# Kernel optimization log

Hardware: AMD Instinct MI355X
Metric: run time of the kernel (lower is better)

The kernel has to match this reference:

```python
import jax, jax.numpy as jnp
import numpy as np

B, S, C = 64, 1024, 512
EPS = 1e-5

def setup_inputs() -> dict:
    key = jax.random.key(0)
    k1, k2, k3 = jax.random.split(key, 3)
    x = jax.random.normal(k1, (B, S, C), dtype=jnp.float32)
    # LayerNorm affine over normalized_shape=[S, C]
    ln_w = jnp.ones((S, C), dtype=jnp.float32)
    ln_b = jnp.zeros((S, C), dtype=jnp.float32)
    # Linear(seq_len, seq_len): torch init U(-1/sqrt(S), 1/sqrt(S))
    bound = 1.0 / np.sqrt(S)
    lin_w = jax.random.uniform(k2, (S, S), jnp.float32, -bound, bound)
    lin_b = jax.random.uniform(k3, (S,), jnp.float32, -bound, bound)
    return {"x": x, "ln_w": ln_w, "ln_b": ln_b, "lin_w": lin_w, "lin_b": lin_b}

def reference(x, ln_w, ln_b, lin_w, lin_b):
    # LayerNorm over last two dims [S, C]
    mu = jnp.mean(x, axis=(1, 2), keepdims=True)
    var = jnp.mean(jnp.square(x - mu), axis=(1, 2), keepdims=True)
    h = (x - mu) * jax.lax.rsqrt(var + EPS) * ln_w + ln_b
    # permute -> [B, C, S], linear over S, relu, permute back, residual
    # fused as einsum over the seq axis directly (no explicit transpose)
    y = jnp.einsum('bsc,ts->btc', h, lin_w) + lin_b[None, :, None]
    y = jax.nn.relu(y)
    return x + y
```

## Files before the change

kernel.cpp:

```cpp
#include <hip/hip_runtime.h>
#include <stdint.h>

#define BB 64
#define SS 1024
#define CC 512
#define EPS 1e-5f

typedef __attribute__((ext_vector_type(8))) __bf16 bf16x8;
typedef __attribute__((ext_vector_type(8))) unsigned short ushort8v;
typedef __attribute__((ext_vector_type(4))) float f32x4;

__device__ __forceinline__ unsigned short f2bf(float f) {
    unsigned int u = __builtin_bit_cast(unsigned int, f);
    u += 0x7fffu + ((u >> 16) & 1u);
    return (unsigned short)(u >> 16);
}

__global__ __launch_bounds__(256) void k_prep(const float* __restrict__ x,
                                              const float* __restrict__ lnw,
                                              const float* __restrict__ lnb,
                                              const float* __restrict__ linw,
                                              unsigned short* __restrict__ Wb,
                                              unsigned short* __restrict__ Ht,
                                              float* __restrict__ psum,
                                              float* __restrict__ psq) {
    const int id = blockIdx.x;
    const int t = threadIdx.x;
    if (id >= 8448) {
        int i = (id - 8448) * 256 + t;
        float4 v = ((const float4*)linw)[i];
        ushort4 o;
        o.x = f2bf(v.x); o.y = f2bf(v.y); o.z = f2bf(v.z); o.w = f2bf(v.w);
        ((ushort4*)Wb)[i] = o;
        return;
    }
    __shared__ uint32_t lds[64 * 33];
    __shared__ float ls[4], lq[4];
    int b, rem;
    const float* src;
    const float* wp;
    if (id < 8192)      { b = id >> 7; rem = id & 127; src = x + (size_t)b * SS * CC; wp = lnw; }
    else if (id < 8320) { b = 64; rem = id - 8192; src = lnw; wp = nullptr; }
    else                { b = 65; rem = id - 8320; src = lnb; wp = nullptr; }
    const int s0 = (rem >> 3) << 6;
    const int c0 = (rem & 7) << 6;
    const int cq = t & 15, spA = t >> 4;
    float sA = 0.f, qA = 0.f;
#pragma unroll
    for (int h = 0; h < 2; ++h) {
        int sp = spA + h * 16;
        int sl = s0 + 2 * sp;
        int cc = c0 + 4 * cq;
        size_t xb = (size_t)sl * CC + cc;
        float4 a0 = *(const float4*)(src + xb);
        float4 a1 = *(const float4*)(src + xb + CC);
        float4 g0 = a0, g1 = a1;
        if (wp) {
            float4 w0 = *(const float4*)(wp + xb);
            float4 w1 = *(const float4*)(wp + xb + CC);
            g0.x = a0.x * w0.x; g0.y = a0.y * w0.y; g0.z = a0.z * w0.z; g0.w = a0.w * w0.w;
            g1.x = a1.x * w1.x; g1.y = a1.y * w1.y; g1.z = a1.z * w1.z; g1.w = a1.w * w1.w;
            sA += a0.x + a0.y + a0.z + a0.w + a1.x + a1.y + a1.z + a1.w;
            qA += a0.x*a0.x + a0.y*a0.y + a0.z*a0.z + a0.w*a0.w
                + a1.x*a1.x + a1.y*a1.y + a1.z*a1.z + a1.w*a1.w;
        }
        uint32_t u0 = (uint32_t)f2bf(g0.x) | ((uint32_t)f2bf(g1.x) << 16);
        uint32_t u1 = (uint32_t)f2bf(g0.y) | ((uint32_t)f2bf(g1.y) << 16);
        uint32_t u2 = (uint32_t)f2bf(g0.z) | ((uint32_t)f2bf(g1.z) << 16);
        uint32_t u3 = (uint32_t)f2bf(g0.w) | ((uint32_t)f2bf(g1.w) << 16);
        lds[(4 * cq + 0) * 33 + sp] = u0;
        lds[(4 * cq + 1) * 33 + sp] = u1;
        lds[(4 * cq + 2) * 33 + sp] = u2;
        lds[(4 * cq + 3) * 33 + sp] = u3;
    }
    if (wp) {
        for (int off = 32; off; off >>= 1) {
            sA += __shfl_down(sA, off, 64);
            qA += __shfl_down(qA, off, 64);
        }
        if ((t & 63) == 0) { ls[t >> 6] = sA; lq[t >> 6] = qA; }
    }
    __syncthreads();
    int spq = t & 7, clA = t >> 3;
#pragma unroll
    for (int h = 0; h < 2; ++h) {
        int cl = clA + h * 32;
        uint4 v;
        v.x = lds[cl * 33 + spq * 4 + 0];
        v.y = lds[cl * 33 + spq * 4 + 1];
        v.z = lds[cl * 33 + spq * 4 + 2];
        v.w = lds[cl * 33 + spq * 4 + 3];
        size_t o = (((size_t)b * CC + c0 + cl) * SS + (size_t)s0 + spq * 8) >> 3;
        ((uint4*)Ht)[o] = v;
    }
    if (wp && t == 0) {
        psum[id] = ls[0] + ls[1] + ls[2] + ls[3];
        psq[id]  = lq[0] + lq[1] + lq[2] + lq[3];
    }
}

__global__ __launch_bounds__(128) void k_stats2(const float* __restrict__ psum,
                                                const float* __restrict__ psq,
                                                float* __restrict__ mu,
                                                float* __restrict__ rsg) {
    int b = blockIdx.x, t = threadIdx.x;
    float s = psum[b * 128 + t];
    float q = psq[b * 128 + t];
    for (int off = 32; off; off >>= 1) {
        s += __shfl_down(s, off, 64);
        q += __shfl_down(q, off, 64);
    }
    __shared__ float ls[2], lq[2];
    if ((t & 63) == 0) { ls[t >> 6] = s; lq[t >> 6] = q; }
    __syncthreads();
    if (t == 0) {
        float ss = ls[0] + ls[1], qq = lq[0] + lq[1];
        const float inv = 1.f / (float)(SS * CC);
        float m = ss * inv;
        float v = qq * inv - m * m;
        mu[b] = m;
        rsg[b] = rsqrtf(v + EPS);
    }
}

template<bool FINAL>
__global__ __launch_bounds__(256) void k_gemm(const unsigned short* __restrict__ A,
                                              const unsigned short* __restrict__ Htall,
                                              const float* __restrict__ x,
                                              const float* __restrict__ linb,
                                              const float* __restrict__ wl,
                                              const float* __restrict__ blp,
                                              const float* __restrict__ muA,
                                              const float* __restrict__ rsA,
                                              float* __restrict__ out) {
    int b, tm, tn;
    if constexpr (FINAL) {
        int wg = ((blockIdx.x & 7) << 8) | (blockIdx.x >> 3);
        b = wg >> 5;
        int r2 = wg & 31;
        tm = r2 >> 2; tn = r2 & 3;
    } else {
        tn = blockIdx.x; tm = blockIdx.y; b = 64 + blockIdx.z;
    }
    __shared__ __align__(16) unsigned short SM[16384];
    const int tid = threadIdx.x;
    const int lane = tid & 63;
    const int w = tid >> 6;
    const int wm = w >> 1, wn = w & 1;
    const int quad = lane >> 4, l15 = lane & 15;

    f32x4 acc[4][4];
#pragma unroll
    for (int mi = 0; mi < 4; ++mi)
#pragma unroll
        for (int ni = 0; ni < 4; ++ni)
            acc[mi][ni] = (f32x4){0.f, 0.f, 0.f, 0.f};

    const unsigned short* Ab = A + (size_t)(tm * 128) * 1024;
    const unsigned short* Bb = Htall + ((size_t)b * 512 + tn * 128) * 1024;
    const int srow = tid >> 2;
    const int scol = (tid & 3) * 8;

    auto stage = [&](int buf, int k0) {
#pragma unroll
        for (int q = 0; q < 2; ++q) {
            __builtin_amdgcn_global_load_lds(
                (const __attribute__((address_space(1))) void*)(Ab + (size_t)(q * 64 + srow) * 1024 + k0 + scol),
                (__attribute__((address_space(3))) void*)(SM + buf * 4096 + q * 2048 + w * 512),
                16, 0, 0);
            __builtin_amdgcn_global_load_lds(
                (const __attribute__((address_space(1))) void*)(Bb + (size_t)(q * 64 + srow) * 1024 + k0 + scol),
                (__attribute__((address_space(3))) void*)(SM + 8192 + buf * 4096 + q * 2048 + w * 512),
                16, 0, 0);
        }
    };
    auto compute = [&](int buf) {
        const unsigned short* as = SM + buf * 4096;
        const unsigned short* bs = SM + 8192 + buf * 4096;
        bf16x8 av[4], bv[4];
#pragma unroll
        for (int i = 0; i < 4; ++i) {
            ushort8v a  = *(const ushort8v*)&as[(wm * 64 + i * 16 + l15) * 32 + quad * 8];
            ushort8v b2 = *(const ushort8v*)&bs[(wn * 64 + i * 16 + l15) * 32 + quad * 8];
            av[i] = __builtin_bit_cast(bf16x8, a);
            bv[i] = __builtin_bit_cast(bf16x8, b2);
        }
#pragma unroll
        for (int mi = 0; mi < 4; ++mi)
#pragma unroll
            for (int ni = 0; ni < 4; ++ni)
                acc[mi][ni] = __builtin_amdgcn_mfma_f32_16x16x32_bf16(
                    av[mi], bv[ni], acc[mi][ni], 0, 0, 0);
    };

    stage(0, 0);
    __syncthreads();
    for (int j = 0; j < 15; ++j) {
        int k0 = j * 64;
        stage(1, k0 + 32);
        compute(0);
        __syncthreads();
        stage(0, k0 + 64);
        compute(1);
        __syncthreads();
    }
    stage(1, 992);
    compute(0);
    __syncthreads();
    compute(1);

    if constexpr (FINAL) {
        __syncthreads();
        const float rsv  = rsA[b];
        const float rsmu = rsv * muA[b];
        float* eps = (float*)SM + (w << 11);
#pragma unroll
        for (int ch = 0; ch < 2; ++ch) {
#pragma unroll
            for (int m2 = 0; m2 < 2; ++m2) {
                int mi = ch * 2 + m2;
#pragma unroll
                for (int ni = 0; ni < 4; ++ni)
#pragma unroll
                    for (int r = 0; r < 4; ++r)
                        eps[(m2 * 16 + quad * 4 + r) * 64 + ni * 16 + l15] = acc[mi][ni][r];
            }
#pragma unroll
            for (int jj = 0; jj < 8; ++jj) {
                int row = jj * 4 + quad;
                int tt = tm * 128 + wm * 64 + ch * 32 + row;
                int cc = tn * 128 + wn * 64 + l15 * 4;
                size_t o2 = (size_t)tt * 512 + cc;
                size_t o  = ((size_t)b * 1024 + tt) * 512 + cc;
                f32x4 v   = *(f32x4*)&eps[row * 64 + l15 * 4];
                f32x4 wv  = *(const f32x4*)&wl[o2];
                f32x4 bv2 = *(const f32x4*)&blp[o2];
                f32x4 xv  = *(const f32x4*)&x[o];
                f32x4 ov;
#pragma unroll
                for (int e = 0; e < 4; ++e) {
                    float vv = rsv * v[e] - rsmu * wv[e] + bv2[e];
                    vv = vv > 0.f ? vv : 0.f;
                    ov[e] = xv[e] + vv;
                }
                *(f32x4*)&out[o] = ov;
            }
        }
    } else {
        int z = b - 64;
#pragma unroll
        for (int mi = 0; mi < 4; ++mi) {
#pragma unroll
            for (int r = 0; r < 4; ++r) {
                int tt = tm * 128 + wm * 64 + mi * 16 + quad * 4 + r;
                float add = z ? linb[tt] : 0.f;
#pragma unroll
                for (int ni = 0; ni < 4; ++ni) {
                    int cc = tn * 128 + wn * 64 + ni * 16 + l15;
                    out[((size_t)z * 1024 + tt) * 512 + cc] = acc[mi][ni][r] + add;
                }
            }
        }
    }
}

extern "C" void kernel_launch(void* const* d_in, const int* in_sizes, int n_in,
                              void* d_out, int out_size, void* d_ws, size_t ws_size,
                              hipStream_t stream) {
    (void)in_sizes; (void)n_in; (void)out_size; (void)ws_size;
    const float* x    = (const float*)d_in[0];
    const float* lnw  = (const float*)d_in[1];
    const float* lnb  = (const float*)d_in[2];
    const float* linw = (const float*)d_in[3];
    const float* linb = (const float*)d_in[4];
    float* out = (float*)d_out;

    char* ws = (char*)d_ws;
    unsigned short* Wb = (unsigned short*)ws;
    unsigned short* Ht = (unsigned short*)(ws + (2u << 20));
    float* wlblp = (float*)(ws + (68u << 20));
    float* psum  = (float*)(ws + (72u << 20));
    float* psq   = psum + 8192;
    float* mu    = psq + 8192;
    float* rsg   = mu + 64;

    k_prep<<<9472, 256, 0, stream>>>(x, lnw, lnb, linw, Wb, Ht, psum, psq);
    k_stats2<<<64, 128, 0, stream>>>(psum, psq, mu, rsg);
    k_gemm<false><<<dim3(4, 8, 2), 256, 0, stream>>>(Wb, Ht, nullptr, linb,
                                                     nullptr, nullptr, nullptr, nullptr, wlblp);
    k_gemm<true><<<2048, 256, 0, stream>>>(Wb, Ht, x, nullptr,
                                           wlblp, wlblp + 512 * 1024, mu, rsg, out);
}
```

Baseline: 395.0 us.

## Triple-buffer GEMM K-loop, swizzle LDS, store epilogue terms in bf16, remap XCD tiles

```diff
diff --git a/kernel.cpp b/kernel.cpp
--- a/kernel.cpp
+++ b/kernel.cpp
@@ -14,6 +14,9 @@
     unsigned int u = __builtin_bit_cast(unsigned int, f);
     u += 0x7fffu + ((u >> 16) & 1u);
     return (unsigned short)(u >> 16);
+}
+__device__ __forceinline__ float bf2f(unsigned short u) {
+    return __builtin_bit_cast(float, (uint32_t)u << 16);
 }
 
 __global__ __launch_bounds__(256) void k_prep(const float* __restrict__ x,
@@ -128,21 +131,22 @@
                                               const unsigned short* __restrict__ Htall,
                                               const float* __restrict__ x,
                                               const float* __restrict__ linb,
-                                              const float* __restrict__ wl,
-                                              const float* __restrict__ blp,
+                                              const unsigned short* __restrict__ wlb,
+                                              const unsigned short* __restrict__ blb,
                                               const float* __restrict__ muA,
                                               const float* __restrict__ rsA,
                                               float* __restrict__ out) {
     int b, tm, tn;
     if constexpr (FINAL) {
-        int wg = ((blockIdx.x & 7) << 8) | (blockIdx.x >> 3);
-        b = wg >> 5;
-        int r2 = wg & 31;
-        tm = r2 >> 2; tn = r2 & 3;
+        int xcd = blockIdx.x & 7;
+        int local = blockIdx.x >> 3;
+        b = xcd * 8 + (local >> 5);
+        tn = (local >> 3) & 3;
+        tm = local & 7;
     } else {
         tn = blockIdx.x; tm = blockIdx.y; b = 64 + blockIdx.z;
     }
-    __shared__ __align__(16) unsigned short SM[16384];
+    __shared__ __align__(16) unsigned short SM[24576];
     const int tid = threadIdx.x;
     const int lane = tid & 63;
     const int w = tid >> 6;
@@ -159,29 +163,30 @@
     const unsigned short* Ab = A + (size_t)(tm * 128) * 1024;
     const unsigned short* Bb = Htall + ((size_t)b * 512 + tn * 128) * 1024;
     const int srow = tid >> 2;
-    const int scol = (tid & 3) * 8;
+    const int scol = ((tid & 3) ^ ((srow >> 1) & 3)) * 8;
 
     auto stage = [&](int buf, int k0) {
 #pragma unroll
         for (int q = 0; q < 2; ++q) {
             __builtin_amdgcn_global_load_lds(
                 (const __attribute__((address_space(1))) void*)(Ab + (size_t)(q * 64 + srow) * 1024 + k0 + scol),
-                (__attribute__((address_space(3))) void*)(SM + buf * 4096 + q * 2048 + w * 512),
+                (__attribute__((address_space(3))) void*)(SM + buf * 8192 + q * 2048 + w * 512),
                 16, 0, 0);
             __builtin_amdgcn_global_load_lds(
                 (const __attribute__((address_space(1))) void*)(Bb + (size_t)(q * 64 + srow) * 1024 + k0 + scol),
-                (__attribute__((address_space(3))) void*)(SM + 8192 + buf * 4096 + q * 2048 + w * 512),
+                (__attribute__((address_space(3))) void*)(SM + buf * 8192 + 4096 + q * 2048 + w * 512),
                 16, 0, 0);
         }
     };
+    const int fs = (l15 >> 1) & 3;
     auto compute = [&](int buf) {
-        const unsigned short* as = SM + buf * 4096;
-        const unsigned short* bs = SM + 8192 + buf * 4096;
+        const unsigned short* as = SM + buf * 8192;
+        const unsigned short* bs = SM + buf * 8192 + 4096;
         bf16x8 av[4], bv[4];
 #pragma unroll
         for (int i = 0; i < 4; ++i) {
-            ushort8v a  = *(const ushort8v*)&as[(wm * 64 + i * 16 + l15) * 32 + quad * 8];
-            ushort8v b2 = *(const ushort8v*)&bs[(wn * 64 + i * 16 + l15) * 32 + quad * 8];
+            ushort8v a  = *(const ushort8v*)&as[(wm * 64 + i * 16 + l15) * 32 + (quad ^ fs) * 8];
+            ushort8v b2 = *(const ushort8v*)&bs[(wn * 64 + i * 16 + l15) * 32 + (quad ^ fs) * 8];
             av[i] = __builtin_bit_cast(bf16x8, a);
             bv[i] = __builtin_bit_cast(bf16x8, b2);
         }
@@ -194,20 +199,21 @@
     };
 
     stage(0, 0);
-    __syncthreads();
-    for (int j = 0; j < 15; ++j) {
-        int k0 = j * 64;
-        stage(1, k0 + 32);
-        compute(0);
-        __syncthreads();
-        stage(0, k0 + 64);
-        compute(1);
-        __syncthreads();
-    }
-    stage(1, 992);
-    compute(0);
-    __syncthreads();
-    compute(1);
+    stage(1, 32);
+    for (int j = 0; j < 31; ++j) {
+        asm volatile("s_waitcnt vmcnt(4)" ::: "memory");
+        __builtin_amdgcn_sched_barrier(0);
+        __builtin_amdgcn_s_barrier();
+        __builtin_amdgcn_sched_barrier(0);
+        int k2 = (j + 2) * 32;
+        if (k2 < 1024) stage((j + 2) % 3, k2);
+        compute(j % 3);
+    }
+    asm volatile("s_waitcnt vmcnt(0)" ::: "memory");
+    __builtin_amdgcn_sched_barrier(0);
+    __builtin_amdgcn_s_barrier();
+    __builtin_amdgcn_sched_barrier(0);
+    compute(31 % 3);
 
     if constexpr (FINAL) {
         __syncthreads();
@@ -232,14 +238,16 @@
                 int cc = tn * 128 + wn * 64 + l15 * 4;
                 size_t o2 = (size_t)tt * 512 + cc;
                 size_t o  = ((size_t)b * 1024 + tt) * 512 + cc;
-                f32x4 v   = *(f32x4*)&eps[row * 64 + l15 * 4];
-                f32x4 wv  = *(const f32x4*)&wl[o2];
-                f32x4 bv2 = *(const f32x4*)&blp[o2];
-                f32x4 xv  = *(const f32x4*)&x[o];
+                f32x4 v    = *(f32x4*)&eps[row * 64 + l15 * 4];
+                ushort4 wv4 = *(const ushort4*)&wlb[o2];
+                ushort4 bv4 = *(const ushort4*)&blb[o2];
+                f32x4 xv   = *(const f32x4*)&x[o];
+                float we[4] = {bf2f(wv4.x), bf2f(wv4.y), bf2f(wv4.z), bf2f(wv4.w)};
+                float be[4] = {bf2f(bv4.x), bf2f(bv4.y), bf2f(bv4.z), bf2f(bv4.w)};
                 f32x4 ov;
 #pragma unroll
                 for (int e = 0; e < 4; ++e) {
-                    float vv = rsv * v[e] - rsmu * wv[e] + bv2[e];
+                    float vv = rsv * v[e] - rsmu * we[e] + be[e];
                     vv = vv > 0.f ? vv : 0.f;
                     ov[e] = xv[e] + vv;
                 }
@@ -248,6 +256,7 @@
         }
     } else {
         int z = b - 64;
+        unsigned short* o16 = (unsigned short*)out;
 #pragma unroll
         for (int mi = 0; mi < 4; ++mi) {
 #pragma unroll
@@ -257,7 +266,7 @@
 #pragma unroll
                 for (int ni = 0; ni < 4; ++ni) {
                     int cc = tn * 128 + wn * 64 + ni * 16 + l15;
-                    out[((size_t)z * 1024 + tt) * 512 + cc] = acc[mi][ni][r] + add;
+                    o16[((size_t)z * 1024 + tt) * 512 + cc] = f2bf(acc[mi][ni][r] + add);
                 }
             }
         }
@@ -276,18 +285,20 @@
     float* out = (float*)d_out;
 
     char* ws = (char*)d_ws;
-    unsigned short* Wb = (unsigned short*)ws;
-    unsigned short* Ht = (unsigned short*)(ws + (2u << 20));
-    float* wlblp = (float*)(ws + (68u << 20));
-    float* psum  = (float*)(ws + (72u << 20));
-    float* psq   = psum + 8192;
-    float* mu    = psq + 8192;
-    float* rsg   = mu + 64;
+    unsigned short* Wb  = (unsigned short*)ws;
+    unsigned short* Ht  = (unsigned short*)(ws + (2u << 20));
+    unsigned short* wlb = (unsigned short*)(ws + (68u << 20));
+    unsigned short* blb = wlb + 512 * 1024;
+    float* psum = (float*)(ws + (72u << 20));
+    float* psq  = psum + 8192;
+    float* mu   = psq + 8192;
+    float* rsg  = mu + 64;
 
     k_prep<<<9472, 256, 0, stream>>>(x, lnw, lnb, linw, Wb, Ht, psum, psq);
     k_stats2<<<64, 128, 0, stream>>>(psum, psq, mu, rsg);
     k_gemm<false><<<dim3(4, 8, 2), 256, 0, stream>>>(Wb, Ht, nullptr, linb,
-                                                     nullptr, nullptr, nullptr, nullptr, wlblp);
+                                                     nullptr, nullptr, nullptr, nullptr,
+                                                     (float*)wlb);
     k_gemm<true><<<2048, 256, 0, stream>>>(Wb, Ht, x, nullptr,
-                                           wlblp, wlblp + 512 * 1024, mu, rsg, out);
-}
+                                           wlb, blb, mu, rsg, out);
+}
```

After: 384.5 us. 2.7% less time.
